# Kernel tuning notes

Measured on AMD Instinct MI355X. Metric: run time of the kernel, lower is better.

## Reference

```python
import jax, jax.numpy as jnp
import numpy as np

B, T, TC, C, CC, H = 2, 2048, 512, 1024, 512, 16
D = C // H  # head dim = 64


def setup_inputs() -> dict:
    key = jax.random.key(0)
    ks = jax.random.split(key, 18)
    w = lambda k, i, o: (jax.random.normal(k, (i, o), jnp.float32) / np.sqrt(i).astype(np.float32))
    return {
        "x": jax.random.normal(ks[0], (B, T, C), jnp.float32),
        "cross_input": jax.random.normal(ks[1], (B, TC, CC), jnp.float32),
        "Wk": w(ks[2], C, C),  "bk": jnp.zeros((C,), jnp.float32),
        "Wq": w(ks[3], C, C),  "bq": jnp.zeros((C,), jnp.float32),
        "Wv": w(ks[4], C, C),  "bv": jnp.zeros((C,), jnp.float32),
        "Wck": w(ks[5], CC, C), "bck": jnp.zeros((C,), jnp.float32),
        "Wcq": w(ks[6], C, C),  "bcq": jnp.zeros((C,), jnp.float32),
        "Wcv": w(ks[7], CC, C), "bcv": jnp.zeros((C,), jnp.float32),
        "Wp": w(ks[8], C, C),   "bp": jnp.zeros((C,), jnp.float32),
    }


def _heads(t):
    # [B, L, C] -> [B, H, L, D]
    b, l, _ = t.shape
    return t.reshape(b, l, H, D).transpose(0, 2, 1, 3)


def reference(x, cross_input, Wk, bk, Wq, bq, Wv, bv, Wck, bck, Wcq, bcq, Wcv, bcv, Wp, bp):
    scale = np.float32(1.0 / np.sqrt(D))
    q = _heads(x @ Wq + bq)
    k = _heads(x @ Wk + bk)
    v = _heads(x @ Wv + bv)
    # causal self-attention with materialized scores (faithful to original)
    att = jnp.einsum("bhqd,bhkd->bhqk", q, k) * scale
    causal = jnp.tril(jnp.ones((T, T), bool))
    att = jnp.where(causal[None, None], att, -jnp.inf)
    y = jnp.einsum("bhqk,bhkd->bhqd", jax.nn.softmax(att, axis=-1), v)
    # cross-attention (no mask)
    qc = _heads(x @ Wcq + bcq)
    kc = _heads(cross_input @ Wck + bck)
    vc = _heads(cross_input @ Wcv + bcv)
    attc = jnp.einsum("bhqd,bhkd->bhqk", qc, kc) * scale
    y = y + jnp.einsum("bhqk,bhkd->bhqd", jax.nn.softmax(attc, axis=-1), vc)
    # merge heads + output projection (dropout prob = 0 -> identity)
    y = y.transpose(0, 2, 1, 3).reshape(x.shape[0], T, C)
    return y @ Wp + bp
```

## Files before the change

### kernel.cpp

```cpp
#include <hip/hip_runtime.h>
#include <hip/hip_bf16.h>
#include <type_traits>

typedef __bf16 bf16;
typedef __bf16 bf16x8 __attribute__((ext_vector_type(8)));
typedef float floatx4 __attribute__((ext_vector_type(4)));

#define QLD 72
#define KLD 136

__device__ __forceinline__ void glds16(const bf16* g, bf16* l) {
  __builtin_amdgcn_global_load_lds((const __attribute__((address_space(1))) void*)g,
                                   (__attribute__((address_space(3))) void*)l, 16, 0, 0);
}

__global__ __launch_bounds__(256) void tobf16_kernel(const float* __restrict__ in,
                                                     bf16* __restrict__ out, int n4) {
  int i = blockIdx.x * 256 + threadIdx.x;
  if (i < n4) {
    float4 f = ((const float4*)in)[i];
    bf16 t[4] = {(bf16)f.x, (bf16)f.y, (bf16)f.z, (bf16)f.w};
    *(uint2*)&out[(long)i * 4] = *(const uint2*)t;
  }
}

__global__ __launch_bounds__(256) void concat4_kernel(float* __restrict__ dst,
                                                      const float* __restrict__ a,
                                                      const float* __restrict__ b,
                                                      const float* __restrict__ c,
                                                      const float* __restrict__ d) {
  int i = blockIdx.x * 256 + threadIdx.x;
  const float* s[4] = {a, b, c, d};
  dst[i] = s[i >> 10][i & 1023];
}

__global__ __launch_bounds__(256) void wtrans_kernel(const float* __restrict__ in,
                                                     bf16* __restrict__ out,
                                                     int R, int C) {
  __shared__ bf16 t[32][33];
  int tx = threadIdx.x, ty = threadIdx.y;
  int c = blockIdx.x * 32 + tx;
#pragma unroll
  for (int i = 0; i < 4; i++) {
    int r = blockIdx.y * 32 + ty + i * 8;
    t[ty + i * 8][tx] = (bf16)in[(long)r * C + c];
  }
  __syncthreads();
  int oc = blockIdx.y * 32 + tx;
#pragma unroll
  for (int i = 0; i < 4; i++) {
    int orr = blockIdx.x * 32 + ty + i * 8;
    out[(long)orr * R + oc] = t[tx][ty + i * 8];
  }
}

template <typename OutT>
__global__ __launch_bounds__(256, 3) void gemm128(const bf16* __restrict__ A,
                                                  const bf16* __restrict__ Bt,
                                                  const float* __restrict__ bias,
                                                  OutT* __restrict__ C,
                                                  int M, int N, int K, int ldc,
                                                  bf16* __restrict__ Vt,
                                                  int vcol0, int vcol1, int Lt, int tok_shift) {
  __shared__ alignas(16) bf16 As[128 * 32];
  __shared__ alignas(16) bf16 Bs[128 * 32];
  const int tid = threadIdx.x, wave = tid >> 6, lane = tid & 63;
  const int l16 = lane & 15, l4 = lane >> 4;
  const int wm = wave & 1, wn = wave >> 1;
  const int n0 = blockIdx.x * 128, m0 = blockIdx.y * 128;
  const int lrow = lane >> 2, lch = (lane & 3) * 8;

  floatx4 acc[4][4];
#pragma unroll
  for (int mt = 0; mt < 4; mt++)
#pragma unroll
    for (int nt = 0; nt < 4; nt++) acc[mt][nt] = (floatx4){0.f, 0.f, 0.f, 0.f};

  const bf16* Ag = A + (long)(m0 + wave * 32 + lrow) * K + lch;
  const bf16* Bg = Bt + (long)(n0 + wave * 32 + lrow) * K + lch;
  bf16* Al = &As[(wave * 32) * 32];
  bf16* Bl = &Bs[(wave * 32) * 32];

  for (int k0 = 0; k0 < K; k0 += 32) {
    __syncthreads();
    glds16(Ag + k0, Al);
    glds16(Ag + k0 + (long)16 * K, Al + 16 * 32);
    glds16(Bg + k0, Bl);
    glds16(Bg + k0 + (long)16 * K, Bl + 16 * 32);
    __syncthreads();
    bf16x8 a[4], b[4];
#pragma unroll
    for (int mt = 0; mt < 4; mt++) a[mt] = *(const bf16x8*)&As[(wm * 64 + mt * 16 + l16) * 32 + l4 * 8];
#pragma unroll
    for (int nt = 0; nt < 4; nt++) b[nt] = *(const bf16x8*)&Bs[(wn * 64 + nt * 16 + l16) * 32 + l4 * 8];
#pragma unroll
    for (int mt = 0; mt < 4; mt++)
#pragma unroll
      for (int nt = 0; nt < 4; nt++)
        acc[mt][nt] = __builtin_amdgcn_mfma_f32_16x16x32_bf16(a[mt], b[nt], acc[mt][nt], 0, 0, 0);
  }

  const bool vpath = (vcol0 >= 0) && (n0 >= vcol0) && (n0 < vcol1);
  if (!vpath) {
    const int coladj = (vcol0 >= 0 && n0 >= vcol1) ? (vcol1 - vcol0) : 0;
#pragma unroll
    for (int nt = 0; nt < 4; nt++) {
      int col = n0 + wn * 64 + nt * 16 + l16;
      float bv = bias[col];
#pragma unroll
      for (int mt = 0; mt < 4; mt++)
#pragma unroll
        for (int r = 0; r < 4; r++) {
          int row = m0 + wm * 64 + mt * 16 + l4 * 4 + r;
          float v = acc[mt][nt][r] + bv;
          if constexpr (std::is_same_v<OutT, float>) C[(long)row * ldc + col - coladj] = v;
          else                                       C[(long)row * ldc + col - coladj] = (bf16)v;
        }
    }
  } else {
#pragma unroll
    for (int nt = 0; nt < 4; nt++) {
      int col = n0 + wn * 64 + nt * 16 + l16;
      int c = col - vcol0, hh = c >> 6, dd = c & 63;
      float bv = bias[col];
#pragma unroll
      for (int mt = 0; mt < 4; mt++) {
        int t0 = m0 + wm * 64 + mt * 16 + l4 * 4;
        int bb = t0 >> tok_shift, t = t0 & ((1 << tok_shift) - 1);
        bf16 tmp[4];
#pragma unroll
        for (int r = 0; r < 4; r++) tmp[r] = (bf16)(acc[mt][nt][r] + bv);
        *(uint2*)&Vt[(((long)bb * 16 + hh) * 64 + dd) * Lt + t] = *(const uint2*)tmp;
      }
    }
  }
}

__global__ __launch_bounds__(256, 2) void attn_kernel(const bf16* __restrict__ QKQc,
                                                      const bf16* __restrict__ VtB,
                                                      const bf16* __restrict__ KcB,
                                                      const bf16* __restrict__ VctB,
                                                      bf16* __restrict__ Y) {
  __shared__ alignas(16) bf16 Qs[64 * QLD];
  __shared__ alignas(16) bf16 Ks[128 * QLD];
  __shared__ alignas(16) bf16 Vts[64 * KLD];
  __shared__ alignas(16) bf16 Ps[64 * KLD];
  const int tid = threadIdx.x, wave = tid >> 6, lane = tid & 63;
  const int l16 = lane & 15, l4 = lane >> 4;
  const int h = blockIdx.y, b = blockIdx.z;

  float o_self[4][4];
  float m_i[4], l_i[4];
  floatx4 oacc[4];

  for (int jj = 0; jj < 2; jj++) {
    const int qt = jj ? (31 - (int)blockIdx.x) : (int)blockIdx.x;
    const int q0 = qt * 64;
    const int qrow0 = q0 + wave * 16 + l4 * 4;

    for (int phase = 0; phase < 2; phase++) {
      const bf16* Qb;
      const bf16* Kb;
      const bf16* Vtb;
      int kstr, vtstr, nkt;
      if (phase == 0) {
        Qb = QKQc + (long)b * 2048 * 3072 + h * 64;
        Kb = Qb + 1024;                      kstr = 3072;
        Vtb = VtB + ((long)b * 16 + h) * 64 * 2048;  vtstr = 2048;
        nkt = (qt + 2) >> 1;
      } else {
        Qb = QKQc + (long)b * 2048 * 3072 + h * 64 + 2048;
        Kb = KcB + (long)b * 512 * 1024 + h * 64;    kstr = 1024;
        Vtb = VctB + ((long)b * 16 + h) * 64 * 512;  vtstr = 512;
        nkt = 4;
      }

      __syncthreads();
#pragma unroll
      for (int i = 0; i < 2; i++) {
        int idx = tid + i * 256, row = idx >> 3, ch = (idx & 7) * 8;
        bf16x8 qv = *(const bf16x8*)(Qb + (long)(q0 + row) * 3072 + ch);
#pragma unroll
        for (int j = 0; j < 8; j++) qv[j] = (bf16)((float)qv[j] * 0.125f);
        *(bf16x8*)&Qs[row * QLD + ch] = qv;
      }
#pragma unroll
      for (int r = 0; r < 4; r++) { m_i[r] = -__builtin_inff(); l_i[r] = 0.f; }
#pragma unroll
      for (int nt = 0; nt < 4; nt++) oacc[nt] = (floatx4){0.f, 0.f, 0.f, 0.f};

      bf16x8 kreg[4], vreg[4];
#pragma unroll
      for (int c = 0; c < 4; c++) {
        int idx = tid + c * 256;
        kreg[c] = *(const bf16x8*)(Kb + (long)(idx >> 3) * kstr + (idx & 7) * 8);
        vreg[c] = *(const bf16x8*)(Vtb + (long)(idx >> 4) * vtstr + (idx & 15) * 8);
      }

      for (int kt = 0; kt < nkt; kt++) {
        const int k0 = kt * 128;
        __syncthreads();
#pragma unroll
        for (int c = 0; c < 4; c++) {
          int idx = tid + c * 256;
          *(bf16x8*)&Ks[(idx >> 3) * QLD + (idx & 7) * 8] = kreg[c];
          *(bf16x8*)&Vts[(idx >> 4) * KLD + (idx & 15) * 8] = vreg[c];
        }
        __syncthreads();
        if (kt + 1 < nkt) {
          const int kn = k0 + 128;
#pragma unroll
          for (int c = 0; c < 4; c++) {
            int idx = tid + c * 256;
            kreg[c] = *(const bf16x8*)(Kb + (long)(kn + (idx >> 3)) * kstr + (idx & 7) * 8);
            vreg[c] = *(const bf16x8*)(Vtb + (long)(idx >> 4) * vtstr + kn + (idx & 15) * 8);
          }
        }

        floatx4 sacc[8];
#pragma unroll
        for (int nt = 0; nt < 8; nt++) sacc[nt] = (floatx4){0.f, 0.f, 0.f, 0.f};
#pragma unroll
        for (int ds = 0; ds < 2; ds++) {
          bf16x8 af = *(const bf16x8*)&Qs[(wave * 16 + l16) * QLD + ds * 32 + l4 * 8];
#pragma unroll
          for (int nt = 0; nt < 8; nt++) {
            bf16x8 bfr = *(const bf16x8*)&Ks[(nt * 16 + l16) * QLD + ds * 32 + l4 * 8];
            sacc[nt] = __builtin_amdgcn_mfma_f32_16x16x32_bf16(af, bfr, sacc[nt], 0, 0, 0);
          }
        }
        if (phase == 0 && kt == nkt - 1) {
          int keyb = k0 + l16;
#pragma unroll
          for (int nt = 0; nt < 8; nt++) {
            int key = keyb + nt * 16;
#pragma unroll
            for (int r = 0; r < 4; r++)
              if (key > qrow0 + r) sacc[nt][r] = -__builtin_inff();
          }
        }
        float mx[4];
#pragma unroll
        for (int r = 0; r < 4; r++) mx[r] = m_i[r];
#pragma unroll
        for (int nt = 0; nt < 8; nt++)
#pragma unroll
          for (int r = 0; r < 4; r++) mx[r] = fmaxf(mx[r], sacc[nt][r]);
#pragma unroll
        for (int r = 0; r < 4; r++) {
#pragma unroll
          for (int off = 1; off < 16; off <<= 1) mx[r] = fmaxf(mx[r], __shfl_xor(mx[r], off));
        }
        float alpha[4], rs[4];
#pragma unroll
        for (int r = 0; r < 4; r++) {
          alpha[r] = __expf(m_i[r] - mx[r]);
          m_i[r] = mx[r];
          rs[r] = 0.f;
        }
#pragma unroll
        for (int nt = 0; nt < 8; nt++)
#pragma unroll
          for (int r = 0; r < 4; r++) {
            float p = __expf(sacc[nt][r] - mx[r]);
            rs[r] += p;
            Ps[(wave * 16 + l4 * 4 + r) * KLD + nt * 16 + l16] = (bf16)p;
          }
#pragma unroll
        for (int r = 0; r < 4; r++) {
#pragma unroll
          for (int off = 1; off < 16; off <<= 1) rs[r] += __shfl_xor(rs[r], off);
          l_i[r] = l_i[r] * alpha[r] + rs[r];
        }
#pragma unroll
        for (int nt = 0; nt < 4; nt++)
#pragma unroll
          for (int r = 0; r < 4; r++) oacc[nt][r] *= alpha[r];
#pragma unroll
        for (int ks = 0; ks < 4; ks++) {
          bf16x8 af = *(const bf16x8*)&Ps[(wave * 16 + l16) * KLD + ks * 32 + l4 * 8];
#pragma unroll
          for (int nt = 0; nt < 4; nt++) {
            bf16x8 bfr = *(const bf16x8*)&Vts[(nt * 16 + l16) * KLD + ks * 32 + l4 * 8];
            oacc[nt] = __builtin_amdgcn_mfma_f32_16x16x32_bf16(af, bfr, oacc[nt], 0, 0, 0);
          }
        }
      }

      if (phase == 0) {
#pragma unroll
        for (int r = 0; r < 4; r++) {
          float inv = 1.0f / l_i[r];
#pragma unroll
          for (int nt = 0; nt < 4; nt++) o_self[nt][r] = oacc[nt][r] * inv;
        }
      } else {
#pragma unroll
        for (int r = 0; r < 4; r++) {
          float inv = 1.0f / l_i[r];
          long row = (long)b * 2048 + q0 + wave * 16 + l4 * 4 + r;
#pragma unroll
          for (int nt = 0; nt < 4; nt++) {
            int col = h * 64 + nt * 16 + l16;
            Y[row * 1024 + col] = (bf16)(o_self[nt][r] + oacc[nt][r] * inv);
          }
        }
      }
    }
  }
}

extern "C" void kernel_launch(void* const* d_in, const int* in_sizes, int n_in,
                              void* d_out, int out_size, void* d_ws, size_t ws_size,
                              hipStream_t stream) {
  const float* x   = (const float*)d_in[0];
  const float* xc  = (const float*)d_in[1];
  const float* Wk  = (const float*)d_in[2];  const float* bk  = (const float*)d_in[3];
  const float* Wq  = (const float*)d_in[4];  const float* bq  = (const float*)d_in[5];
  const float* Wv  = (const float*)d_in[6];  const float* bv  = (const float*)d_in[7];
  const float* Wck = (const float*)d_in[8];  const float* bck = (const float*)d_in[9];
  const float* Wcq = (const float*)d_in[10]; const float* bcq = (const float*)d_in[11];
  const float* Wcv = (const float*)d_in[12]; const float* bcv = (const float*)d_in[13];
  const float* Wp  = (const float*)d_in[14]; const float* bp  = (const float*)d_in[15];

  char* ws = (char*)d_ws;
  const size_t MB = 1ull << 20;
  bf16*  WT_all = (bf16*)(ws + 0);
  bf16*  WC_all = (bf16*)(ws + 8 * MB);
  bf16*  WpT    = (bf16*)(ws + 10 * MB);
  bf16*  xbf    = (bf16*)(ws + 12 * MB);
  bf16*  Yb     = xbf;
  bf16*  xcbf   = (bf16*)(ws + 20 * MB);
  float* bias4  = (float*)(ws + 21 * MB);
  float* biasc  = (float*)(ws + 21 * MB + 65536);
  bf16*  QKQc   = (bf16*)(ws + 22 * MB);
  bf16*  VtB    = (bf16*)(ws + 46 * MB);
  bf16*  KcB    = (bf16*)(ws + 54 * MB);
  bf16*  VctB   = (bf16*)(ws + 56 * MB);

  tobf16_kernel<<<4096, 256, 0, stream>>>(x, xbf, 1048576);
  tobf16_kernel<<<512, 256, 0, stream>>>(xc, xcbf, 131072);

  dim3 tb(32, 8);
  wtrans_kernel<<<dim3(32, 32), tb, 0, stream>>>(Wq,  WT_all + 0ll * 1024 * 1024, 1024, 1024);
  wtrans_kernel<<<dim3(32, 32), tb, 0, stream>>>(Wk,  WT_all + 1ll * 1024 * 1024, 1024, 1024);
  wtrans_kernel<<<dim3(32, 32), tb, 0, stream>>>(Wv,  WT_all + 2ll * 1024 * 1024, 1024, 1024);
  wtrans_kernel<<<dim3(32, 32), tb, 0, stream>>>(Wcq, WT_all + 3ll * 1024 * 1024, 1024, 1024);
  wtrans_kernel<<<dim3(32, 16), tb, 0, stream>>>(Wck, WC_all + 0ll * 1024 * 512, 512, 1024);
  wtrans_kernel<<<dim3(32, 16), tb, 0, stream>>>(Wcv, WC_all + 1ll * 1024 * 512, 512, 1024);
  wtrans_kernel<<<dim3(32, 32), tb, 0, stream>>>(Wp,  WpT, 1024, 1024);

  concat4_kernel<<<16, 256, 0, stream>>>(bias4, bq, bk, bv, bcq);
  concat4_kernel<<<8, 256, 0, stream>>>(biasc, bck, bcv, bck, bcv);

  gemm128<bf16><<<dim3(32, 32), 256, 0, stream>>>(xbf, WT_all, bias4, QKQc,
                                                  4096, 4096, 1024, 3072,
                                                  VtB, 2048, 3072, 2048, 11);
  gemm128<bf16><<<dim3(16, 8), 256, 0, stream>>>(xcbf, WC_all, biasc, KcB,
                                                 1024, 2048, 512, 1024,
                                                 VctB, 1024, 2048, 512, 9);

  attn_kernel<<<dim3(16, 16, 2), 256, 0, stream>>>(QKQc, VtB, KcB, VctB, Yb);

  gemm128<float><<<dim3(8, 32), 256, 0, stream>>>(Yb, WpT, bp, (float*)d_out,
                                                  4096, 1024, 1024, 1024,
                                                  nullptr, -1, -1, 0, 0);
}
```

Before: 292.9 us.

## Keep Q in registers, raise attention occupancy, use exp2, fuse prep kernels

The attention kernel now loads each wave's pre-scaled Q fragments straight into registers, so the Q shared-memory tile is gone. Less LDS per block allows launch bounds to rise from 2 to 3 blocks per CU. The softmax scale now folds in log2(e), so the exponentials use the hardware exp2 builtin instead of __expf. The eleven preprocessing launches (bf16 casts, bias concatenation, weight transposes) are merged into one prep kernel that branches on block index, cutting launch overhead. The risks are more register pressure under the tighter occupancy target and uncoalesced Q loads straight from global memory.

```diff
diff --git a/kernel.cpp b/kernel.cpp
--- a/kernel.cpp
+++ b/kernel.cpp
@@ -9,48 +9,64 @@
 #define QLD 72
 #define KLD 136
 
+#if __has_builtin(__builtin_amdgcn_exp2f)
+#define EXP2(x) __builtin_amdgcn_exp2f(x)
+#else
+#define EXP2(x) exp2f(x)
+#endif
+
 __device__ __forceinline__ void glds16(const bf16* g, bf16* l) {
   __builtin_amdgcn_global_load_lds((const __attribute__((address_space(1))) void*)g,
                                    (__attribute__((address_space(3))) void*)l, 16, 0, 0);
 }
 
-__global__ __launch_bounds__(256) void tobf16_kernel(const float* __restrict__ in,
-                                                     bf16* __restrict__ out, int n4) {
-  int i = blockIdx.x * 256 + threadIdx.x;
-  if (i < n4) {
-    float4 f = ((const float4*)in)[i];
+struct PrepArgs {
+  const float* x; const float* xc;
+  bf16* xbf; bf16* xcbf;
+  const float* b4[4];
+  const float* bc[2];
+  float* bias4; float* biasc;
+  const float* W[7];
+  bf16* WT[7];
+};
+
+__global__ __launch_bounds__(256) void prep_kernel(PrepArgs a) {
+  __shared__ bf16 tsh[32][33];
+  const int bx = blockIdx.x, tid = threadIdx.x;
+  if (bx < 4096) {
+    int i = bx * 256 + tid;
+    float4 f = ((const float4*)a.x)[i];
     bf16 t[4] = {(bf16)f.x, (bf16)f.y, (bf16)f.z, (bf16)f.w};
-    *(uint2*)&out[(long)i * 4] = *(const uint2*)t;
-  }
-}
-
-__global__ __launch_bounds__(256) void concat4_kernel(float* __restrict__ dst,
-                                                      const float* __restrict__ a,
-                                                      const float* __restrict__ b,
-                                                      const float* __restrict__ c,
-                                                      const float* __restrict__ d) {
-  int i = blockIdx.x * 256 + threadIdx.x;
-  const float* s[4] = {a, b, c, d};
-  dst[i] = s[i >> 10][i & 1023];
-}
-
-__global__ __launch_bounds__(256) void wtrans_kernel(const float* __restrict__ in,
-                                                     bf16* __restrict__ out,
-                                                     int R, int C) {
-  __shared__ bf16 t[32][33];
-  int tx = threadIdx.x, ty = threadIdx.y;
-  int c = blockIdx.x * 32 + tx;
-#pragma unroll
-  for (int i = 0; i < 4; i++) {
-    int r = blockIdx.y * 32 + ty + i * 8;
-    t[ty + i * 8][tx] = (bf16)in[(long)r * C + c];
-  }
-  __syncthreads();
-  int oc = blockIdx.y * 32 + tx;
-#pragma unroll
-  for (int i = 0; i < 4; i++) {
-    int orr = blockIdx.x * 32 + ty + i * 8;
-    out[(long)orr * R + oc] = t[tx][ty + i * 8];
+    *(uint2*)&a.xbf[(long)i * 4] = *(const uint2*)t;
+  } else if (bx < 4608) {
+    int i = (bx - 4096) * 256 + tid;
+    float4 f = ((const float4*)a.xc)[i];
+    bf16 t[4] = {(bf16)f.x, (bf16)f.y, (bf16)f.z, (bf16)f.w};
+    *(uint2*)&a.xcbf[(long)i * 4] = *(const uint2*)t;
+  } else if (bx < 4632) {
+    int lb = bx - 4608;
+    if (lb < 16) { int i = lb * 256 + tid; a.bias4[i] = a.b4[i >> 10][i & 1023]; }
+    else         { int i = (lb - 16) * 256 + tid; a.biasc[i] = a.bc[i >> 10][i & 1023]; }
+  } else {
+    int t = bx - 4632, w, R, bxw, byw;
+    if (t < 5120) { w = t >> 10; R = 1024; int l = t & 1023; bxw = l & 31; byw = l >> 5; }
+    else { int t2 = t - 5120; w = 5 + (t2 >> 9); R = 512; int l = t2 & 511; bxw = l & 31; byw = l >> 5; }
+    const float* in = a.W[w];
+    bf16* out = a.WT[w];
+    int tx = tid & 31, ty = tid >> 5;
+    int c = bxw * 32 + tx;
+#pragma unroll
+    for (int i = 0; i < 4; i++) {
+      int r = byw * 32 + ty + i * 8;
+      tsh[ty + i * 8][tx] = (bf16)in[(long)r * 1024 + c];
+    }
+    __syncthreads();
+    int oc = byw * 32 + tx;
+#pragma unroll
+    for (int i = 0; i < 4; i++) {
+      int orr = bxw * 32 + ty + i * 8;
+      out[(long)orr * R + oc] = tsh[tx][ty + i * 8];
+    }
   }
 }
 
@@ -136,12 +152,11 @@
   }
 }
 
-__global__ __launch_bounds__(256, 2) void attn_kernel(const bf16* __restrict__ QKQc,
+__global__ __launch_bounds__(256, 3) void attn_kernel(const bf16* __restrict__ QKQc,
                                                       const bf16* __restrict__ VtB,
                                                       const bf16* __restrict__ KcB,
                                                       const bf16* __restrict__ VctB,
                                                       bf16* __restrict__ Y) {
-  __shared__ alignas(16) bf16 Qs[64 * QLD];
   __shared__ alignas(16) bf16 Ks[128 * QLD];
   __shared__ alignas(16) bf16 Vts[64 * KLD];
   __shared__ alignas(16) bf16 Ps[64 * KLD];
@@ -165,7 +180,7 @@
       int kstr, vtstr, nkt;
       if (phase == 0) {
         Qb = QKQc + (long)b * 2048 * 3072 + h * 64;
-        Kb = Qb + 1024;                      kstr = 3072;
+        Kb = Qb + 1024;                              kstr = 3072;
         Vtb = VtB + ((long)b * 16 + h) * 64 * 2048;  vtstr = 2048;
         nkt = (qt + 2) >> 1;
       } else {
@@ -175,14 +190,16 @@
         nkt = 4;
       }
 
-      __syncthreads();
-#pragma unroll
-      for (int i = 0; i < 2; i++) {
-        int idx = tid + i * 256, row = idx >> 3, ch = (idx & 7) * 8;
-        bf16x8 qv = *(const bf16x8*)(Qb + (long)(q0 + row) * 3072 + ch);
-#pragma unroll
-        for (int j = 0; j < 8; j++) qv[j] = (bf16)((float)qv[j] * 0.125f);
-        *(bf16x8*)&Qs[row * QLD + ch] = qv;
+      bf16x8 qf[2];
+      {
+        const bf16* qp = Qb + (long)(q0 + wave * 16 + l16) * 3072 + l4 * 8;
+#pragma unroll
+        for (int ds = 0; ds < 2; ds++) {
+          bf16x8 v = *(const bf16x8*)(qp + ds * 32);
+#pragma unroll
+          for (int j = 0; j < 8; j++) v[j] = (bf16)((float)v[j] * 0.18033688f);
+          qf[ds] = v;
+        }
       }
 #pragma unroll
       for (int r = 0; r < 4; r++) { m_i[r] = -__builtin_inff(); l_i[r] = 0.f; }
@@ -222,11 +239,10 @@
         for (int nt = 0; nt < 8; nt++) sacc[nt] = (floatx4){0.f, 0.f, 0.f, 0.f};
 #pragma unroll
         for (int ds = 0; ds < 2; ds++) {
-          bf16x8 af = *(const bf16x8*)&Qs[(wave * 16 + l16) * QLD + ds * 32 + l4 * 8];
 #pragma unroll
           for (int nt = 0; nt < 8; nt++) {
             bf16x8 bfr = *(const bf16x8*)&Ks[(nt * 16 + l16) * QLD + ds * 32 + l4 * 8];
-            sacc[nt] = __builtin_amdgcn_mfma_f32_16x16x32_bf16(af, bfr, sacc[nt], 0, 0, 0);
+            sacc[nt] = __builtin_amdgcn_mfma_f32_16x16x32_bf16(qf[ds], bfr, sacc[nt], 0, 0, 0);
           }
         }
         if (phase == 0 && kt == nkt - 1) {
@@ -254,7 +270,7 @@
         float alpha[4], rs[4];
 #pragma unroll
         for (int r = 0; r < 4; r++) {
-          alpha[r] = __expf(m_i[r] - mx[r]);
+          alpha[r] = EXP2(m_i[r] - mx[r]);
           m_i[r] = mx[r];
           rs[r] = 0.f;
         }
@@ -262,7 +278,7 @@
         for (int nt = 0; nt < 8; nt++)
 #pragma unroll
           for (int r = 0; r < 4; r++) {
-            float p = __expf(sacc[nt][r] - mx[r]);
+            float p = EXP2(sacc[nt][r] - mx[r]);
             rs[r] += p;
             Ps[(wave * 16 + l4 * 4 + r) * KLD + nt * 16 + l16] = (bf16)p;
           }
@@ -298,7 +314,7 @@
 #pragma unroll
         for (int r = 0; r < 4; r++) {
           float inv = 1.0f / l_i[r];
-          long row = (long)b * 2048 + q0 + wave * 16 + l4 * 4 + r;
+          long row = (long)b * 2048 + qrow0 + r;
 #pragma unroll
           for (int nt = 0; nt < 4; nt++) {
             int col = h * 64 + nt * 16 + l16;
@@ -338,20 +354,19 @@
   bf16*  KcB    = (bf16*)(ws + 54 * MB);
   bf16*  VctB   = (bf16*)(ws + 56 * MB);
 
-  tobf16_kernel<<<4096, 256, 0, stream>>>(x, xbf, 1048576);
-  tobf16_kernel<<<512, 256, 0, stream>>>(xc, xcbf, 131072);
-
-  dim3 tb(32, 8);
-  wtrans_kernel<<<dim3(32, 32), tb, 0, stream>>>(Wq,  WT_all + 0ll * 1024 * 1024, 1024, 1024);
-  wtrans_kernel<<<dim3(32, 32), tb, 0, stream>>>(Wk,  WT_all + 1ll * 1024 * 1024, 1024, 1024);
-  wtrans_kernel<<<dim3(32, 32), tb, 0, stream>>>(Wv,  WT_all + 2ll * 1024 * 1024, 1024, 1024);
-  wtrans_kernel<<<dim3(32, 32), tb, 0, stream>>>(Wcq, WT_all + 3ll * 1024 * 1024, 1024, 1024);
-  wtrans_kernel<<<dim3(32, 16), tb, 0, stream>>>(Wck, WC_all + 0ll * 1024 * 512, 512, 1024);
-  wtrans_kernel<<<dim3(32, 16), tb, 0, stream>>>(Wcv, WC_all + 1ll * 1024 * 512, 512, 1024);
-  wtrans_kernel<<<dim3(32, 32), tb, 0, stream>>>(Wp,  WpT, 1024, 1024);
-
-  concat4_kernel<<<16, 256, 0, stream>>>(bias4, bq, bk, bv, bcq);
-  concat4_kernel<<<8, 256, 0, stream>>>(biasc, bck, bcv, bck, bcv);
+  PrepArgs pa;
+  pa.x = x; pa.xc = xc; pa.xbf = xbf; pa.xcbf = xcbf;
+  pa.b4[0] = bq; pa.b4[1] = bk; pa.b4[2] = bv; pa.b4[3] = bcq;
+  pa.bc[0] = bck; pa.bc[1] = bcv;
+  pa.bias4 = bias4; pa.biasc = biasc;
+  pa.W[0] = Wq;  pa.WT[0] = WT_all + 0ll * 1024 * 1024;
+  pa.W[1] = Wk;  pa.WT[1] = WT_all + 1ll * 1024 * 1024;
+  pa.W[2] = Wv;  pa.WT[2] = WT_all + 2ll * 1024 * 1024;
+  pa.W[3] = Wcq; pa.WT[3] = WT_all + 3ll * 1024 * 1024;
+  pa.W[4] = Wp;  pa.WT[4] = WpT;
+  pa.W[5] = Wck; pa.WT[5] = WC_all + 0ll * 1024 * 512;
+  pa.W[6] = Wcv; pa.WT[6] = WC_all + 1ll * 1024 * 512;
+  prep_kernel<<<10776, 256, 0, stream>>>(pa);
 
   gemm128<bf16><<<dim3(32, 32), 256, 0, stream>>>(xbf, WT_all, bias4, QKQc,
                                                   4096, 4096, 1024, 3072,
```

Result: no change. 288.6 us (-1.5%).
